# Performance work log

Hardware: AMD Instinct MI355X
Metric: run time of the kernel (lower is better)

## Reference

```python
import jax, jax.numpy as jnp
import numpy as np

SRC_SIZE = 1024
TGT_SIZE = 1024
ATT_SIZE = 1024
S, T, B = 1024, 1024, 32


def setup_inputs() -> dict:
    key = jax.random.key(0)
    k1, k2, k3, k4 = jax.random.split(key, 4)
    source = jax.random.normal(k1, (S, B, SRC_SIZE), dtype=jnp.float32)
    target = jax.random.normal(k2, (T, B, TGT_SIZE), dtype=jnp.float32)
    # nn.Linear(in, out, bias=False): weight shape (out, in), y = x @ W.T
    scale1 = 1.0 / np.sqrt(SRC_SIZE)
    scale2 = 1.0 / np.sqrt(TGT_SIZE)
    W1 = jax.random.uniform(k3, (ATT_SIZE, SRC_SIZE), dtype=jnp.float32, minval=-scale1, maxval=scale1)
    W2 = jax.random.uniform(k4, (ATT_SIZE, TGT_SIZE), dtype=jnp.float32, minval=-scale2, maxval=scale2)
    return {"source": source, "target": target, "W1": W1, "W2": W2}


def reference(source, target, W1, W2):
    # Transform into attention space: (S,B,A) and (T,B,A)
    ts = jnp.einsum('sbd,ad->sba', source, W1)
    tt = jnp.einsum('tbd,ad->tba', target, W2)
    # Multiplicative scores: (S,T,B) = sum_a ts[s,b,a]*tt[t,b,a]
    scores = jnp.einsum('sba,tba->stb', ts, tt)
    # Softmax over source positions (axis 0)
    weights = jax.nn.softmax(scores, axis=0)  # (S,T,B)
    # Attention vectors: (T,B,src_size) = sum_s weights[s,t,b]*source[s,b,d]
    return jnp.einsum('stb,sbd->tbd', weights, source)
```

## Files before the change

### kernel.cpp

```cpp
#include <hip/hip_runtime.h>
#include <hip/hip_bf16.h>

typedef _Float16 half_t;
typedef __attribute__((ext_vector_type(8))) _Float16 half8;
typedef __attribute__((ext_vector_type(4))) _Float16 half4;
typedef __attribute__((ext_vector_type(4))) float floatx4;
typedef __attribute__((ext_vector_type(4))) float f32x4;

#define DEVFN static __device__ __forceinline__

DEVFN void gll16(const void* g, void* l) {
    __builtin_amdgcn_global_load_lds(
        (const __attribute__((address_space(1))) unsigned int*)g,
        (__attribute__((address_space(3))) unsigned int*)l, 16, 0, 0);
}
DEVFN f32x4 mfma16(half8 a, half8 b, f32x4 c) {
    return __builtin_amdgcn_mfma_f32_16x16x32_f16(a, b, c, 0, 0, 0);
}
DEVFN void vm0() { asm volatile("s_waitcnt vmcnt(0)" ::: "memory"); __builtin_amdgcn_sched_barrier(0); }
DEVFN void vm4() { asm volatile("s_waitcnt vmcnt(4)" ::: "memory"); __builtin_amdgcn_sched_barrier(0); }
DEVFN void bar() { __builtin_amdgcn_s_barrier(); __builtin_amdgcn_sched_barrier(0); }

__global__ __launch_bounds__(256) void cvt_f16(
    const float* __restrict__ in, half_t* __restrict__ out, int n4)
{
    int i = blockIdx.x * 256 + threadIdx.x;
    if (i >= n4) return;
    floatx4 v = ((const floatx4*)in)[i];
    half4 h;
#pragma unroll
    for (int j = 0; j < 4; j++) h[j] = (half_t)v[j];
    ((half4*)out)[i] = h;
}

__global__ __launch_bounds__(256) void transpose_src_f16(
    const float* __restrict__ src, half_t* __restrict__ srcT, half_t* __restrict__ srcH)
{
    __shared__ float tile[32][33];
    int s0 = blockIdx.x << 5, d0 = blockIdx.y << 5, b = blockIdx.z;
    int t = threadIdx.x;
    int si = t >> 3, dj = (t & 7) << 2;
    floatx4 v = *(const floatx4*)&src[((size_t)(s0 + si) * 32 + b) * 1024 + d0 + dj];
    tile[si][dj + 0] = v[0]; tile[si][dj + 1] = v[1];
    tile[si][dj + 2] = v[2]; tile[si][dj + 3] = v[3];
    half4 hv;
#pragma unroll
    for (int j = 0; j < 4; j++) hv[j] = (half_t)v[j];
    *(half4*)&srcH[((size_t)(s0 + si) * 32 + b) * 1024 + d0 + dj] = hv;
    __syncthreads();
    int di = t >> 3, sj = (t & 7) << 2;
    half4 o;
#pragma unroll
    for (int q = 0; q < 4; q++) o[q] = (half_t)tile[sj + q][di];
    *(half4*)&srcT[((size_t)b * 1024 + d0 + di) * 1024 + s0 + sj] = o;
}

template <bool OUT_F16>
__global__ __launch_bounds__(512, 2) void gemm256(
    const half_t* __restrict__ A, const half_t* __restrict__ B,
    void* __restrict__ Cv,
    int lda, int ldb, int ldc, int K,
    long long bA, long long bB, long long bC,
    int gx, int gy)
{
    __shared__ char lds[131072];
    const int nwg = gridDim.x;
    const int bid = blockIdx.x;
    const int sw = (bid & 7) * (nwg >> 3) + (bid >> 3);
    const int x = sw % gx;
    const int r1 = sw / gx;
    const int y = r1 % gy;
    const int z = r1 / gy;

    const int t = threadIdx.x, lane = t & 63, w = t >> 6;
    const int wr = w >> 2, wc = w & 3;
    const int m0 = y << 8, n0 = x << 8;
    const half_t* pA = A + (size_t)bA * z + (size_t)m0 * lda;
    const half_t* pB = B + (size_t)bB * z + (size_t)n0 * ldb;

    int srow[2], scol[2];
#pragma unroll
    for (int i = 0; i < 2; i++) {
        int slot = (w << 7) + (i << 6) + lane;
        srow[i] = slot >> 2;
        scol[i] = (slot & 3) << 3;
    }
    const unsigned stOff = (unsigned)((w << 7) << 4);

    const int lr = lane & 15, q = lane >> 4;
    const unsigned aRd = (unsigned)((((wr << 7) + lr) << 6) + (q << 4));
    const unsigned bRd = 65536u + (unsigned)((((wc << 6) + lr) << 6) + (q << 4));

    f32x4 acc[8][4];
#pragma unroll
    for (int m = 0; m < 8; m++)
#pragma unroll
        for (int n = 0; n < 4; n++) acc[m][n] = (f32x4){0.f, 0.f, 0.f, 0.f};

    auto stA = [&](int nb, int kh, int kc) {
#pragma unroll
        for (int i = 0; i < 2; i++)
            gll16(pA + (size_t)srow[i] * lda + (kc + kh * 32 + scol[i]),
                  lds + (nb << 15) + (kh << 14) + stOff + (i << 10));
    };
    auto stB = [&](int nb, int kh, int kc) {
#pragma unroll
        for (int i = 0; i < 2; i++)
            gll16(pB + (size_t)srow[i] * ldb + (kc + kh * 32 + scol[i]),
                  lds + 65536 + (nb << 15) + (kh << 14) + stOff + (i << 10));
    };

    stA(0, 0, 0); stB(0, 0, 0); stA(0, 1, 0); stB(0, 1, 0);

    half8 av_a[4], av_b[4], bv0[4], bv1[4];
    const int NT = K >> 6;
    for (int tt = 0; tt < NT; ++tt) {
        const int buf = tt & 1, nb = buf ^ 1;
        const bool st = (tt + 1 < NT);
        const int kn = (tt + 1) << 6;
        const unsigned b0 = (unsigned)(buf << 15);
        const unsigned b1 = b0 + 16384u;

        vm4();
        bar();
        if (st) stA(nb, 0, kn);
#pragma unroll
        for (int m = 0; m < 4; m++) av_a[m] = *(const half8*)(lds + b0 + aRd + m * 1024);
#pragma unroll
        for (int n = 0; n < 4; n++) bv0[n] = *(const half8*)(lds + b0 + bRd + n * 1024);
#pragma unroll
        for (int m = 0; m < 4; m++) av_b[m] = *(const half8*)(lds + b0 + aRd + (4 + m) * 1024);
        __builtin_amdgcn_s_setprio(1);
#pragma unroll
        for (int m = 0; m < 4; m++)
#pragma unroll
            for (int n = 0; n < 4; n++)
                acc[m][n] = mfma16(av_a[m], bv0[n], acc[m][n]);
        __builtin_amdgcn_s_setprio(0);
        if (st) stB(nb, 0, kn);

        if (st) vm4(); else vm0();
        bar();
#pragma unroll
        for (int m = 0; m < 4; m++) av_a[m] = *(const half8*)(lds + b1 + aRd + m * 1024);
#pragma unroll
        for (int n = 0; n < 4; n++) bv1[n] = *(const half8*)(lds + b1 + bRd + n * 1024);
        __builtin_amdgcn_s_setprio(1);
#pragma unroll
        for (int m = 0; m < 4; m++)
#pragma unroll
            for (int n = 0; n < 4; n++)
                acc[4 + m][n] = mfma16(av_b[m], bv0[n], acc[4 + m][n]);
        __builtin_amdgcn_s_setprio(0);
        if (st) stA(nb, 1, kn);
#pragma unroll
        for (int m = 0; m < 4; m++) av_b[m] = *(const half8*)(lds + b1 + aRd + (4 + m) * 1024);
        __builtin_amdgcn_s_setprio(1);
#pragma unroll
        for (int m = 0; m < 4; m++)
#pragma unroll
            for (int n = 0; n < 4; n++)
                acc[m][n] = mfma16(av_a[m], bv1[n], acc[m][n]);
        __builtin_amdgcn_s_setprio(0);
        if (st) stB(nb, 1, kn);
        __builtin_amdgcn_s_setprio(1);
#pragma unroll
        for (int m = 0; m < 4; m++)
#pragma unroll
            for (int n = 0; n < 4; n++)
                acc[4 + m][n] = mfma16(av_b[m], bv1[n], acc[4 + m][n]);
        __builtin_amdgcn_s_setprio(0);
    }

    const size_t zC = (size_t)bC * z;
    const int r0 = m0 + (wr << 7) + (q << 2);
    const int c0 = n0 + (wc << 6) + lr;
#pragma unroll
    for (int m = 0; m < 8; m++)
#pragma unroll
        for (int fn = 0; fn < 4; fn++)
#pragma unroll
            for (int j = 0; j < 4; j++) {
                size_t idx = zC + (size_t)(r0 + m * 16 + j) * ldc + (c0 + fn * 16);
                if constexpr (OUT_F16)
                    ((half_t*)Cv)[idx] = (half_t)acc[m][fn][j];
                else
                    ((float*)Cv)[idx] = acc[m][fn][j];
            }
}

__global__ __launch_bounds__(256) void softmax_k(
    const float* __restrict__ sc, half_t* __restrict__ wt)
{
    size_t row = blockIdx.x;
    const floatx4* p = (const floatx4*)(sc + row * 1024);
    int t = threadIdx.x, lane = t & 63, w = t >> 6;
    floatx4 v = p[t];
    float m = fmaxf(fmaxf(v[0], v[1]), fmaxf(v[2], v[3]));
#pragma unroll
    for (int o = 1; o < 64; o <<= 1) m = fmaxf(m, __shfl_xor(m, o));
    __shared__ float red[8];
    if (lane == 0) red[w] = m;
    __syncthreads();
    m = fmaxf(fmaxf(red[0], red[1]), fmaxf(red[2], red[3]));
    floatx4 e;
#pragma unroll
    for (int j = 0; j < 4; j++) e[j] = __expf(v[j] - m);
    float s = e[0] + e[1] + e[2] + e[3];
#pragma unroll
    for (int o = 1; o < 64; o <<= 1) s += __shfl_xor(s, o);
    if (lane == 0) red[4 + w] = s;
    __syncthreads();
    s = red[4] + red[5] + red[6] + red[7];
    float inv = 1.0f / s;
    half4 o4;
#pragma unroll
    for (int j = 0; j < 4; j++) o4[j] = (half_t)(e[j] * inv);
    ((half4*)(wt + row * 1024))[t] = o4;
}

extern "C" void kernel_launch(void* const* d_in, const int* in_sizes, int n_in,
                              void* d_out, int out_size, void* d_ws, size_t ws_size,
                              hipStream_t stream)
{
    const float* src = (const float*)d_in[0];
    const float* tgt = (const float*)d_in[1];
    const float* W1  = (const float*)d_in[2];
    const float* W2  = (const float*)d_in[3];
    float* out = (float*)d_out;

    char* ws = (char*)d_ws;
    const size_t MB = 1024ull * 1024ull;
    half_t* srcH  = (half_t*)(ws);
    half_t* tgtH  = (half_t*)(ws + 64  * MB);
    half_t* tsH   = (half_t*)(ws + 128 * MB);
    half_t* ttH   = (half_t*)(ws + 192 * MB);
    half_t* srcT  = (half_t*)(ws + 256 * MB);
    float*  scores= (float*) (ws + 320 * MB);
    half_t* w1h   = (half_t*)(ws + 448 * MB);
    half_t* w2h   = (half_t*)(ws + 450 * MB);
    half_t* wts   = srcH;

    cvt_f16<<<32768, 256, 0, stream>>>(tgt, tgtH, 8388608);
    cvt_f16<<<1024, 256, 0, stream>>>(W1, w1h, 262144);
    cvt_f16<<<1024, 256, 0, stream>>>(W2, w2h, 262144);
    transpose_src_f16<<<dim3(32, 32, 32), 256, 0, stream>>>(src, srcT, srcH);

    gemm256<true><<<512, 512, 0, stream>>>(srcH, w1h, tsH,
        1024, 1024, 1024, 1024, 0ll, 0ll, 0ll, 4, 128);
    gemm256<true><<<512, 512, 0, stream>>>(tgtH, w2h, ttH,
        1024, 1024, 1024, 1024, 0ll, 0ll, 0ll, 4, 128);

    gemm256<false><<<512, 512, 0, stream>>>(ttH, tsH, scores,
        32768, 32768, 1024, 1024, 1024ll, 1024ll, 1024ll * 1024ll, 4, 4);

    softmax_k<<<32768, 256, 0, stream>>>(scores, wts);

    gemm256<false><<<512, 512, 0, stream>>>(wts, srcT, out,
        1024, 1024, 32768, 1024, 1024ll * 1024ll, 1024ll * 1024ll, 1024ll, 4, 4);
}
```

Measured before the change: 701.1 us.

## Fold W1 and W2 into a single Gram matrix and store scores in fp16

The two projection GEMMs are replaced by one small GEMM that computes G = W2^T W1 from transposed weights, followed by one large GEMM that computes u = target·G. Scores are then u·source^T, which removes a full 32-batch 1024x1024x1024 projection GEMM. Scores are also written as fp16, and the softmax runs in place on them, which halves score memory traffic. The cost is more fp16 rounding: G and the scores both lose precision, and large score values could overflow or lose accuracy in fp16.

```diff
diff --git a/kernel.cpp b/kernel.cpp
--- a/kernel.cpp
+++ b/kernel.cpp
@@ -31,6 +31,24 @@
 #pragma unroll
     for (int j = 0; j < 4; j++) h[j] = (half_t)v[j];
     ((half4*)out)[i] = h;
+}
+
+__global__ __launch_bounds__(256) void transpose_w(
+    const float* __restrict__ w, half_t* __restrict__ wt)
+{
+    __shared__ float tile[32][33];
+    int a0 = blockIdx.x << 5, d0 = blockIdx.y << 5;
+    int t = threadIdx.x;
+    int ai = t >> 3, dj = (t & 7) << 2;
+    floatx4 v = *(const floatx4*)&w[(size_t)(a0 + ai) * 1024 + d0 + dj];
+    tile[ai][dj + 0] = v[0]; tile[ai][dj + 1] = v[1];
+    tile[ai][dj + 2] = v[2]; tile[ai][dj + 3] = v[3];
+    __syncthreads();
+    int di = t >> 3, aj = (t & 7) << 2;
+    half4 o;
+#pragma unroll
+    for (int q = 0; q < 4; q++) o[q] = (half_t)tile[aj + q][di];
+    *(half4*)&wt[(size_t)(d0 + di) * 1024 + a0 + aj] = o;
 }
 
 __global__ __launch_bounds__(256) void transpose_src_f16(
@@ -189,13 +207,15 @@
             }
 }
 
-__global__ __launch_bounds__(256) void softmax_k(
-    const float* __restrict__ sc, half_t* __restrict__ wt)
+__global__ __launch_bounds__(256) void softmax_h(half_t* __restrict__ sc)
 {
     size_t row = blockIdx.x;
-    const floatx4* p = (const floatx4*)(sc + row * 1024);
+    half_t* p = sc + row * 1024;
     int t = threadIdx.x, lane = t & 63, w = t >> 6;
-    floatx4 v = p[t];
+    half4 v4 = ((const half4*)p)[t];
+    float v[4];
+#pragma unroll
+    for (int j = 0; j < 4; j++) v[j] = (float)v4[j];
     float m = fmaxf(fmaxf(v[0], v[1]), fmaxf(v[2], v[3]));
 #pragma unroll
     for (int o = 1; o < 64; o <<= 1) m = fmaxf(m, __shfl_xor(m, o));
@@ -203,7 +223,7 @@
     if (lane == 0) red[w] = m;
     __syncthreads();
     m = fmaxf(fmaxf(red[0], red[1]), fmaxf(red[2], red[3]));
-    floatx4 e;
+    float e[4];
 #pragma unroll
     for (int j = 0; j < 4; j++) e[j] = __expf(v[j] - m);
     float s = e[0] + e[1] + e[2] + e[3];
@@ -216,7 +236,7 @@
     half4 o4;
 #pragma unroll
     for (int j = 0; j < 4; j++) o4[j] = (half_t)(e[j] * inv);
-    ((half4*)(wt + row * 1024))[t] = o4;
+    ((half4*)p)[t] = o4;
 }
 
 extern "C" void kernel_launch(void* const* d_in, const int* in_sizes, int n_in,
@@ -231,31 +251,31 @@
 
     char* ws = (char*)d_ws;
     const size_t MB = 1024ull * 1024ull;
-    half_t* srcH  = (half_t*)(ws);
-    half_t* tgtH  = (half_t*)(ws + 64  * MB);
-    half_t* tsH   = (half_t*)(ws + 128 * MB);
-    half_t* ttH   = (half_t*)(ws + 192 * MB);
-    half_t* srcT  = (half_t*)(ws + 256 * MB);
-    float*  scores= (float*) (ws + 320 * MB);
-    half_t* w1h   = (half_t*)(ws + 448 * MB);
-    half_t* w2h   = (half_t*)(ws + 450 * MB);
-    half_t* wts   = srcH;
-
+    half_t* srcH    = (half_t*)(ws);
+    half_t* tgtH    = (half_t*)(ws + 64  * MB);
+    half_t* uH      = (half_t*)(ws + 128 * MB);
+    half_t* srcT    = (half_t*)(ws + 192 * MB);
+    half_t* scoresH = (half_t*)(ws + 256 * MB);
+    half_t* w1t     = (half_t*)(ws + 320 * MB);
+    half_t* w2t     = (half_t*)(ws + 322 * MB);
+    half_t* G       = (half_t*)(ws + 324 * MB);
+
+    transpose_w<<<dim3(32, 32), 256, 0, stream>>>(W1, w1t);
+    transpose_w<<<dim3(32, 32), 256, 0, stream>>>(W2, w2t);
     cvt_f16<<<32768, 256, 0, stream>>>(tgt, tgtH, 8388608);
-    cvt_f16<<<1024, 256, 0, stream>>>(W1, w1h, 262144);
-    cvt_f16<<<1024, 256, 0, stream>>>(W2, w2h, 262144);
     transpose_src_f16<<<dim3(32, 32, 32), 256, 0, stream>>>(src, srcT, srcH);
 
-    gemm256<true><<<512, 512, 0, stream>>>(srcH, w1h, tsH,
+    gemm256<true><<<16, 512, 0, stream>>>(w1t, w2t, G,
+        1024, 1024, 1024, 1024, 0ll, 0ll, 0ll, 4, 4);
+
+    gemm256<true><<<512, 512, 0, stream>>>(tgtH, G, uH,
         1024, 1024, 1024, 1024, 0ll, 0ll, 0ll, 4, 128);
-    gemm256<true><<<512, 512, 0, stream>>>(tgtH, w2h, ttH,
-        1024, 1024, 1024, 1024, 0ll, 0ll, 0ll, 4, 128);
-
-    gemm256<false><<<512, 512, 0, stream>>>(ttH, tsH, scores,
+
+    gemm256<true><<<512, 512, 0, stream>>>(uH, srcH, scoresH,
         32768, 32768, 1024, 1024, 1024ll, 1024ll, 1024ll * 1024ll, 4, 4);
 
-    softmax_k<<<32768, 256, 0, stream>>>(scores, wts);
-
-    gemm256<false><<<512, 512, 0, stream>>>(wts, srcT, out,
+    softmax_h<<<32768, 256, 0, stream>>>(scoresH);
+
+    gemm256<false><<<512, 512, 0, stream>>>(scoresH, srcT, out,
         1024, 1024, 32768, 1024, 1024ll * 1024ll, 1024ll * 1024ll, 1024ll, 4, 4);
 }
```

After: 632.4 us. 1.11x faster.
